# Kernel optimization log

Measured on AMD Instinct MI355X. Metric: run time of the kernel, lower is better.

## Reference

```python
import jax, jax.numpy as jnp
from jax import lax
import numpy as np

VOCAB, EMBED, HIDDEN, MEL = 256, 256, 1024, 80


def lstm_seq(x_seq, Wih, Whh, bih, bhh):
    """x_seq: [T, B, in]; returns hidden sequence [T, B, H]. PyTorch gate order i,f,g,o."""
    H = Whh.shape[1]
    B = x_seq.shape[1]
    b = bih + bhh

    def step(carry, x):
        h, c = carry
        g = x @ Wih.T + h @ Whh.T + b  # [B, 4H]
        i, f, gg, o = jnp.split(g, 4, axis=-1)
        c = jax.nn.sigmoid(f) * c + jax.nn.sigmoid(i) * jnp.tanh(gg)
        h = jax.nn.sigmoid(o) * jnp.tanh(c)
        return (h, c), h

    init = (jnp.zeros((B, H), x_seq.dtype), jnp.zeros((B, H), x_seq.dtype))
    _, ys = lax.scan(step, init, x_seq)
    return ys


def setup_inputs() -> dict:
    key = jax.random.key(0)
    ks = jax.random.split(key, 13)
    s_h = 1.0 / np.sqrt(HIDDEN)
    u = lambda k, shape, s: jax.random.uniform(k, shape, jnp.float32, -s, s)
    return {
        "text": jax.random.randint(ks[0], (64, 1024), 0, VOCAB),
        "text_lens": jax.random.randint(ks[1], (64,), 1, 1024),
        "max_audio_len": 1000,
        "W_emb": jax.random.normal(ks[2], (VOCAB, EMBED), jnp.float32),
        "enc_Wih": u(ks[3], (4 * HIDDEN, EMBED), s_h),
        "enc_Whh": u(ks[4], (4 * HIDDEN, HIDDEN), s_h),
        "enc_bih": u(ks[5], (4 * HIDDEN,), s_h),
        "enc_bhh": u(ks[6], (4 * HIDDEN,), s_h),
        "dec_Wih": u(ks[7], (4 * HIDDEN, MEL), s_h),
        "dec_Whh": u(ks[8], (4 * HIDDEN, HIDDEN), s_h),
        "dec_bih": u(ks[9], (4 * HIDDEN,), s_h),
        "dec_bhh": u(ks[10], (4 * HIDDEN,), s_h),
        "lin_W": u(ks[11], (MEL, HIDDEN), s_h),
        "lin_b": u(ks[12], (MEL,), s_h),
    }


def reference(text, text_lens, max_audio_len, W_emb, enc_Wih, enc_Whh, enc_bih,
              enc_bhh, dec_Wih, dec_Whh, dec_bih, dec_bhh, lin_W, lin_b):
    B = text.shape[0]
    # Encoder over text (output unused downstream, but computed as in the original).
    emb = W_emb[text]                      # [B, T, E]
    enc_out = lstm_seq(emb.transpose(1, 0, 2), enc_Wih, enc_Whh, enc_bih, enc_bhh)
    enc_out = enc_out.transpose(1, 0, 2)   # [B, T, H]

    b_dec = dec_bih + dec_bhh

    def dec_step(carry, _):
        h, c, x = carry                    # x: [B, MEL] previous frame
        g = x @ dec_Wih.T + h @ dec_Whh.T + b_dec
        i, f, gg, o = jnp.split(g, 4, axis=-1)
        c = jax.nn.sigmoid(f) * c + jax.nn.sigmoid(i) * jnp.tanh(gg)
        h = jax.nn.sigmoid(o) * jnp.tanh(c)
        frame = h @ lin_W.T + lin_b        # [B, MEL]
        return (h, c, frame), frame

    init = (jnp.zeros((B, HIDDEN), jnp.float32),
            jnp.zeros((B, HIDDEN), jnp.float32),
            jnp.zeros((B, MEL), jnp.float32))
    _, frames = lax.scan(dec_step, init, None, length=max_audio_len)
    return frames.transpose(1, 0, 2)       # [B, max_audio_len, MEL]
```

## Files before the change

kernel.cpp:

```cpp
#include <hip/hip_runtime.h>
#include <math.h>

#define HIDDEN 1024
#define MEL    80
#define TSTEPS 1000
#define BATCH  64

#define NBLK 64
#define TPB  1024

typedef unsigned long long ull;

__device__ __forceinline__ float sigm_f(float x) { return 1.0f / (1.0f + __expf(-x)); }
__device__ __forceinline__ float tanh_f(float x) { return 1.0f - 2.0f / (1.0f + __expf(2.0f * x)); }

__device__ __forceinline__ unsigned int pack_h(float h, int tag) {
    int q = (int)rintf(h * 8388608.0f);
    q = max(-8388607, min(8388607, q));
    return ((unsigned int)(tag & 0xFF) << 24) | ((unsigned int)q & 0xFFFFFFu);
}
__device__ __forceinline__ float unpack_h(unsigned int v) {
    int q = ((int)(v << 8)) >> 8;
    return (float)q * 1.1920928955078125e-7f;
}

__global__ __launch_bounds__(TPB, 4) void tts_recur(
    const float* __restrict__ dec_Wih,
    const float* __restrict__ dec_Whh,
    const float* __restrict__ dec_bih,
    const float* __restrict__ dec_bhh,
    const float* __restrict__ lin_W,
    const float* __restrict__ lin_b,
    float* __restrict__ h_hist,
    unsigned int* __restrict__ hbuf)
{
    const int tid  = threadIdx.x;
    const int blk  = blockIdx.x;
    const int wv   = tid >> 6;
    const int lane = tid & 63;
    const int jj   = lane & 15;
    const int gate = lane >> 4;
    const int unit_g = blk * 16 + jj;
    const int row_g  = gate * HIDDEN + unit_g;

    if (wv == 0) __builtin_amdgcn_s_setprio(3);

    __shared__ __align__(16) float hEx[16][64];
    __shared__ float part[2][64 * 17];

    const float* wih = dec_Wih + (size_t)row_g * MEL;
    const float* whh = dec_Whh + (size_t)row_g * HIDDEN + wv * 64;
    float4 w[16];
#pragma unroll
    for (int k = 0; k < 16; ++k)
        w[k] = *(const float4*)(whh + k * 4);
#pragma unroll 1
    for (int m = 0; m < MEL; ++m) {
        const float aw = wih[m];
        const float4* lw4 = (const float4*)(lin_W + (size_t)m * HIDDEN + wv * 64);
#pragma unroll
        for (int k = 0; k < 8; ++k) {
            const float4 lw = lw4[k];
            w[k].x = fmaf(aw, lw.x, w[k].x); w[k].y = fmaf(aw, lw.y, w[k].y);
            w[k].z = fmaf(aw, lw.z, w[k].z); w[k].w = fmaf(aw, lw.w, w[k].w);
        }
#pragma unroll
        for (int k = 8; k < 16; ++k) {
            const float4 lw = lw4[k];
            w[k].x = fmaf(aw, lw.x, w[k].x); w[k].y = fmaf(aw, lw.y, w[k].y);
            w[k].z = fmaf(aw, lw.z, w[k].z); w[k].w = fmaf(aw, lw.w, w[k].w);
        }
    }
    float b_comb_r = dec_bih[row_g] + dec_bhh[row_g];
    const float b_dec_r = b_comb_r;
    for (int m = 0; m < MEL; ++m)
        b_comb_r = fmaf(wih[m], lin_b[m], b_comb_r);

    float c_prev = 0.0f;

    if (wv == 0) {
        const float g = b_dec_r;
        const float gi = __shfl(g, jj, 64);
        const float gg = __shfl(g, 32 + jj, 64);
        const float go = __shfl(g, 48 + jj, 64);
        const float c  = sigm_f(gi) * tanh_f(gg);
        const float h  = sigm_f(go) * tanh_f(c);
        c_prev = c;
        if (lane < 16) {
            __hip_atomic_store(hbuf + unit_g, pack_h(h, 1),
                               __ATOMIC_RELAXED, __HIP_MEMORY_SCOPE_AGENT);
            h_hist[unit_g] = h;
        }
    }

    for (int t = 1; t < TSTEPS; ++t) {
        const int buf = t & 1;
        {
            const unsigned int* src = hbuf + ((t - 1) & 1) * HIDDEN;
            const unsigned int want = (unsigned int)t & 0xFFu;
            unsigned int v = __hip_atomic_load(src + tid, __ATOMIC_RELAXED, __HIP_MEMORY_SCOPE_AGENT);
            while ((v >> 24) != want)
                v = __hip_atomic_load(src + tid, __ATOMIC_RELAXED, __HIP_MEMORY_SCOPE_AGENT);
            hEx[wv][lane] = unpack_h(v);
        }
        __builtin_amdgcn_wave_barrier();

        const float4* hp = (const float4*)&hEx[wv][0];
        float a0 = 0.f, a1 = 0.f, a2 = 0.f, a3 = 0.f;
#pragma unroll
        for (int k = 0; k < 16; k += 4) {
            const float4 h0 = hp[k], h1 = hp[k + 1], h2 = hp[k + 2], h3 = hp[k + 3];
            a0 = fmaf(w[k].x, h0.x, a0);   a0 = fmaf(w[k].y, h0.y, a0);
            a0 = fmaf(w[k].z, h0.z, a0);   a0 = fmaf(w[k].w, h0.w, a0);
            a1 = fmaf(w[k+1].x, h1.x, a1); a1 = fmaf(w[k+1].y, h1.y, a1);
            a1 = fmaf(w[k+1].z, h1.z, a1); a1 = fmaf(w[k+1].w, h1.w, a1);
            a2 = fmaf(w[k+2].x, h2.x, a2); a2 = fmaf(w[k+2].y, h2.y, a2);
            a2 = fmaf(w[k+2].z, h2.z, a2); a2 = fmaf(w[k+2].w, h2.w, a2);
            a3 = fmaf(w[k+3].x, h3.x, a3); a3 = fmaf(w[k+3].y, h3.y, a3);
            a3 = fmaf(w[k+3].w, h3.w, a3); a3 = fmaf(w[k+3].z, h3.z, a3);
        }
        part[buf][lane * 17 + wv] = (a0 + a1) + (a2 + a3);
        __syncthreads();

        if (wv == 0) {
            const float* pr = &part[buf][lane * 17];
            float p[16];
#pragma unroll
            for (int i = 0; i < 16; ++i) p[i] = pr[i];
            const float s = (((p[0]+p[1])+(p[2]+p[3])) + ((p[4]+p[5])+(p[6]+p[7])))
                          + (((p[8]+p[9])+(p[10]+p[11])) + ((p[12]+p[13])+(p[14]+p[15])));
            const float g = s + b_comb_r;
            const float gi = __shfl(g, jj, 64);
            const float gf = __shfl(g, 16 + jj, 64);
            const float gg = __shfl(g, 32 + jj, 64);
            const float go = __shfl(g, 48 + jj, 64);
            const float c  = sigm_f(gf) * c_prev + sigm_f(gi) * tanh_f(gg);
            const float h  = sigm_f(go) * tanh_f(c);
            c_prev = c;
            if (lane < 16) {
                __hip_atomic_store(hbuf + buf * HIDDEN + unit_g, pack_h(h, t + 1),
                                   __ATOMIC_RELAXED, __HIP_MEMORY_SCOPE_AGENT);
                h_hist[(size_t)t * HIDDEN + unit_g] = h;
            }
        }
    }
}

__global__ __launch_bounds__(128) void tts_frames(
    const float* __restrict__ lin_W, const float* __restrict__ lin_b,
    const float* __restrict__ h_hist, float* __restrict__ out)
{
    const int t = blockIdx.x;
    const int tid = threadIdx.x;
    __shared__ __align__(16) float h_sh[HIDDEN];
    __shared__ float f_s[MEL];
    const float4* src = (const float4*)(h_hist + (size_t)t * HIDDEN);
    ((float4*)h_sh)[tid] = src[tid];
    ((float4*)h_sh)[tid + 128] = src[tid + 128];
    __syncthreads();
    if (tid < MEL) {
        const float* wrow = lin_W + (size_t)tid * HIDDEN;
        float acc = lin_b[tid];
#pragma unroll 8
        for (int c = 0; c < HIDDEN; ++c)
            acc = fmaf(wrow[c], h_sh[c], acc);
        f_s[tid] = acc;
    }
    __syncthreads();
    for (int idx = tid; idx < BATCH * MEL; idx += 128) {
        const int b = idx / MEL;
        const int m = idx - b * MEL;
        out[(size_t)b * TSTEPS * MEL + (size_t)t * MEL + m] = f_s[m];
    }
}

extern "C" void kernel_launch(void* const* d_in, const int* in_sizes, int n_in,
                              void* d_out, int out_size, void* d_ws, size_t ws_size,
                              hipStream_t stream) {
    const float* dec_Wih = (const float*)d_in[8];
    const float* dec_Whh = (const float*)d_in[9];
    const float* dec_bih = (const float*)d_in[10];
    const float* dec_bhh = (const float*)d_in[11];
    const float* lin_W   = (const float*)d_in[12];
    const float* lin_b   = (const float*)d_in[13];
    float* out = (float*)d_out;

    float* h_hist = (float*)d_ws;
    unsigned int* hbuf = (unsigned int*)((char*)d_ws + (size_t)TSTEPS * HIDDEN * sizeof(float));

    hipLaunchKernelGGL(tts_recur, dim3(NBLK), dim3(TPB), 0, stream,
                       dec_Wih, dec_Whh, dec_bih, dec_bhh, lin_W, lin_b, h_hist, hbuf);
    hipLaunchKernelGGL(tts_frames, dim3(TSTEPS), dim3(128), 0, stream,
                       lin_W, lin_b, h_hist, out);
}
```

Before: 2.304 ms.

## Split recurrent LSTM across 256 small blocks with 4 units each

Repartitions the persistent recurrent kernel from 64 blocks of 1024 threads (16 hidden units each) to 256 blocks of 256 threads (4 units each). Each thread still holds 64 Whh weights in registers, but each wave now covers 256 columns across 4 sub-groups. The h exchange now loads 4 packed values per thread via two 64-bit atomic loads into a padded shared buffer. The aim is to spread the work over more CUs and to shrink the per-block barrier and reduction. The cost is more blocks polling global memory for the tagged h values every step, which adds cross-block sync traffic.

```diff
diff --git a/kernel.cpp b/kernel.cpp
--- a/kernel.cpp
+++ b/kernel.cpp
@@ -6,8 +6,9 @@
 #define TSTEPS 1000
 #define BATCH  64
 
-#define NBLK 64
-#define TPB  1024
+#define NBLK 256
+#define TPB  256
+#define UPB  4
 
 typedef unsigned long long ull;
 
@@ -19,12 +20,14 @@
     q = max(-8388607, min(8388607, q));
     return ((unsigned int)(tag & 0xFF) << 24) | ((unsigned int)q & 0xFFFFFFu);
 }
-__device__ __forceinline__ float unpack_h(unsigned int v) {
+__device__ __forceinline__ float unpack_u(unsigned int v) {
     int q = ((int)(v << 8)) >> 8;
     return (float)q * 1.1920928955078125e-7f;
 }
 
-__global__ __launch_bounds__(TPB, 4) void tts_recur(
+__device__ __forceinline__ int hoff(int col) { return col + ((col >> 6) << 2); }
+
+__global__ __launch_bounds__(TPB) void tts_recur(
     const float* __restrict__ dec_Wih,
     const float* __restrict__ dec_Whh,
     const float* __restrict__ dec_bih,
@@ -38,18 +41,19 @@
     const int blk  = blockIdx.x;
     const int wv   = tid >> 6;
     const int lane = tid & 63;
-    const int jj   = lane & 15;
-    const int gate = lane >> 4;
-    const int unit_g = blk * 16 + jj;
-    const int row_g  = gate * HIDDEN + unit_g;
+    const int sub  = lane >> 4;
+    const int r16  = lane & 15;
+    const int unit0 = blk * UPB;
+    const int row_g = (r16 >> 2) * HIDDEN + unit0 + (r16 & 3);
+    const int colbase = wv * 256 + sub * 64;
 
     if (wv == 0) __builtin_amdgcn_s_setprio(3);
 
-    __shared__ __align__(16) float hEx[16][64];
-    __shared__ float part[2][64 * 17];
+    __shared__ __align__(16) float hEx[HIDDEN + 64];
+    __shared__ float part[2][16 * 17];
 
     const float* wih = dec_Wih + (size_t)row_g * MEL;
-    const float* whh = dec_Whh + (size_t)row_g * HIDDEN + wv * 64;
+    const float* whh = dec_Whh + (size_t)row_g * HIDDEN + colbase;
     float4 w[16];
 #pragma unroll
     for (int k = 0; k < 16; ++k)
@@ -57,7 +61,7 @@
 #pragma unroll 1
     for (int m = 0; m < MEL; ++m) {
         const float aw = wih[m];
-        const float4* lw4 = (const float4*)(lin_W + (size_t)m * HIDDEN + wv * 64);
+        const float4* lw4 = (const float4*)(lin_W + (size_t)m * HIDDEN + colbase);
 #pragma unroll
         for (int k = 0; k < 8; ++k) {
             const float4 lw = lw4[k];
@@ -80,32 +84,44 @@
 
     if (wv == 0) {
         const float g = b_dec_r;
-        const float gi = __shfl(g, jj, 64);
-        const float gg = __shfl(g, 32 + jj, 64);
-        const float go = __shfl(g, 48 + jj, 64);
+        const int j = lane & 3;
+        const float gi = __shfl(g, j, 64);
+        const float gg = __shfl(g, 8 + j, 64);
+        const float go = __shfl(g, 12 + j, 64);
         const float c  = sigm_f(gi) * tanh_f(gg);
         const float h  = sigm_f(go) * tanh_f(c);
         c_prev = c;
-        if (lane < 16) {
-            __hip_atomic_store(hbuf + unit_g, pack_h(h, 1),
+        if (lane < 4) {
+            __hip_atomic_store(hbuf + unit0 + lane, pack_h(h, 1),
                                __ATOMIC_RELAXED, __HIP_MEMORY_SCOPE_AGENT);
-            h_hist[unit_g] = h;
+            h_hist[unit0 + lane] = h;
         }
     }
 
     for (int t = 1; t < TSTEPS; ++t) {
         const int buf = t & 1;
         {
-            const unsigned int* src = hbuf + ((t - 1) & 1) * HIDDEN;
+            const ull* src = (const ull*)(hbuf + ((t - 1) & 1) * HIDDEN) + tid * 2;
             const unsigned int want = (unsigned int)t & 0xFFu;
-            unsigned int v = __hip_atomic_load(src + tid, __ATOMIC_RELAXED, __HIP_MEMORY_SCOPE_AGENT);
-            while ((v >> 24) != want)
-                v = __hip_atomic_load(src + tid, __ATOMIC_RELAXED, __HIP_MEMORY_SCOPE_AGENT);
-            hEx[wv][lane] = unpack_h(v);
+            ull a = __hip_atomic_load(src,     __ATOMIC_RELAXED, __HIP_MEMORY_SCOPE_AGENT);
+            ull b = __hip_atomic_load(src + 1, __ATOMIC_RELAXED, __HIP_MEMORY_SCOPE_AGENT);
+            while ((((unsigned)(a >> 24)) & 0xFFu) != want ||
+                   ((unsigned)(a >> 56))          != want ||
+                   (((unsigned)(b >> 24)) & 0xFFu) != want ||
+                   ((unsigned)(b >> 56))          != want) {
+                a = __hip_atomic_load(src,     __ATOMIC_RELAXED, __HIP_MEMORY_SCOPE_AGENT);
+                b = __hip_atomic_load(src + 1, __ATOMIC_RELAXED, __HIP_MEMORY_SCOPE_AGENT);
+            }
+            float4 hv;
+            hv.x = unpack_u((unsigned)a);
+            hv.y = unpack_u((unsigned)(a >> 32));
+            hv.z = unpack_u((unsigned)b);
+            hv.w = unpack_u((unsigned)(b >> 32));
+            *(float4*)&hEx[hoff(tid * 4)] = hv;
         }
         __builtin_amdgcn_wave_barrier();
 
-        const float4* hp = (const float4*)&hEx[wv][0];
+        const float4* hp = (const float4*)&hEx[hoff(colbase)];
         float a0 = 0.f, a1 = 0.f, a2 = 0.f, a3 = 0.f;
 #pragma unroll
         for (int k = 0; k < 16; k += 4) {
@@ -117,30 +133,34 @@
             a2 = fmaf(w[k+2].x, h2.x, a2); a2 = fmaf(w[k+2].y, h2.y, a2);
             a2 = fmaf(w[k+2].z, h2.z, a2); a2 = fmaf(w[k+2].w, h2.w, a2);
             a3 = fmaf(w[k+3].x, h3.x, a3); a3 = fmaf(w[k+3].y, h3.y, a3);
-            a3 = fmaf(w[k+3].w, h3.w, a3); a3 = fmaf(w[k+3].z, h3.z, a3);
-        }
-        part[buf][lane * 17 + wv] = (a0 + a1) + (a2 + a3);
+            a3 = fmaf(w[k+3].z, h3.z, a3); a3 = fmaf(w[k+3].w, h3.w, a3);
+        }
+        part[buf][r16 * 17 + (wv * 4 + sub)] = (a0 + a1) + (a2 + a3);
         __syncthreads();
 
         if (wv == 0) {
-            const float* pr = &part[buf][lane * 17];
-            float p[16];
-#pragma unroll
-            for (int i = 0; i < 16; ++i) p[i] = pr[i];
-            const float s = (((p[0]+p[1])+(p[2]+p[3])) + ((p[4]+p[5])+(p[6]+p[7])))
-                          + (((p[8]+p[9])+(p[10]+p[11])) + ((p[12]+p[13])+(p[14]+p[15])));
-            const float g = s + b_comb_r;
-            const float gi = __shfl(g, jj, 64);
-            const float gf = __shfl(g, 16 + jj, 64);
-            const float gg = __shfl(g, 32 + jj, 64);
-            const float go = __shfl(g, 48 + jj, 64);
+            float g = 0.0f;
+            if (lane < 16) {
+                const float* pr = &part[buf][lane * 17];
+                float p[16];
+#pragma unroll
+                for (int i = 0; i < 16; ++i) p[i] = pr[i];
+                const float s = (((p[0]+p[1])+(p[2]+p[3])) + ((p[4]+p[5])+(p[6]+p[7])))
+                              + (((p[8]+p[9])+(p[10]+p[11])) + ((p[12]+p[13])+(p[14]+p[15])));
+                g = s + b_comb_r;
+            }
+            const int j = lane & 3;
+            const float gi = __shfl(g, j, 64);
+            const float gf = __shfl(g, 4 + j, 64);
+            const float gg = __shfl(g, 8 + j, 64);
+            const float go = __shfl(g, 12 + j, 64);
             const float c  = sigm_f(gf) * c_prev + sigm_f(gi) * tanh_f(gg);
             const float h  = sigm_f(go) * tanh_f(c);
             c_prev = c;
-            if (lane < 16) {
-                __hip_atomic_store(hbuf + buf * HIDDEN + unit_g, pack_h(h, t + 1),
+            if (lane < 4) {
+                __hip_atomic_store(hbuf + buf * HIDDEN + unit0 + lane, pack_h(h, t + 1),
                                    __ATOMIC_RELAXED, __HIP_MEMORY_SCOPE_AGENT);
-                h_hist[(size_t)t * HIDDEN + unit_g] = h;
+                h_hist[(size_t)t * HIDDEN + unit0 + lane] = h;
             }
         }
     }
```

Result: slower. 3.174 ms (+37.7%).

## Repartition recurrence to 32 blocks of 32 units with register+LDS weight split

Applied to the files above, without the earlier changes.

Restructures the persistent recurrence kernel. Instead of 64 blocks of 1024 threads each owning 16 units, it launches 256 blocks, keeps only every eighth one alive (32 active blocks), and gives each 512-thread block 32 hidden units. Each thread covers one gate row and a 256-column slice, holding 192 weights in registers and 64 in LDS. The hidden-state poll now uses two 64-bit loads per lane, and the final reduction is over 4 partials instead of 16. The aim is fewer cross-block synchronisation participants and fewer reduction partials per step. In exchange there is more per-thread serial FMA work per step, higher register pressure, and extra idle blocks that launch and exit immediately.

```diff
diff --git a/kernel.cpp b/kernel.cpp
--- a/kernel.cpp
+++ b/kernel.cpp
@@ -6,8 +6,11 @@
 #define TSTEPS 1000
 #define BATCH  64
 
-#define NBLK 64
-#define TPB  1024
+#define NBLK 256
+#define TPB  512
+#define UPB  32
+#define VREG 48
+#define LCH  16
 
 typedef unsigned long long ull;
 
@@ -19,12 +22,12 @@
     q = max(-8388607, min(8388607, q));
     return ((unsigned int)(tag & 0xFF) << 24) | ((unsigned int)q & 0xFFFFFFu);
 }
-__device__ __forceinline__ float unpack_h(unsigned int v) {
+__device__ __forceinline__ float unpack_u(unsigned int v) {
     int q = ((int)(v << 8)) >> 8;
     return (float)q * 1.1920928955078125e-7f;
 }
 
-__global__ __launch_bounds__(TPB, 4) void tts_recur(
+__global__ __launch_bounds__(TPB, 2) void tts_recur(
     const float* __restrict__ dec_Wih,
     const float* __restrict__ dec_Whh,
     const float* __restrict__ dec_bih,
@@ -34,82 +37,120 @@
     float* __restrict__ h_hist,
     unsigned int* __restrict__ hbuf)
 {
+    if (blockIdx.x & 7) return;
+    const int W    = blockIdx.x >> 3;
     const int tid  = threadIdx.x;
-    const int blk  = blockIdx.x;
     const int wv   = tid >> 6;
     const int lane = tid & 63;
-    const int jj   = lane & 15;
-    const int gate = lane >> 4;
-    const int unit_g = blk * 16 + jj;
-    const int row_g  = gate * HIDDEN + unit_g;
-
-    if (wv == 0) __builtin_amdgcn_s_setprio(3);
-
-    __shared__ __align__(16) float hEx[16][64];
-    __shared__ float part[2][64 * 17];
-
-    const float* wih = dec_Wih + (size_t)row_g * MEL;
-    const float* whh = dec_Whh + (size_t)row_g * HIDDEN + wv * 64;
-    float4 w[16];
-#pragma unroll
-    for (int k = 0; k < 16; ++k)
-        w[k] = *(const float4*)(whh + k * 4);
+    const int row  = tid & 127;
+    const int cg   = tid >> 7;
+    const int unit0 = W * UPB;
+    const int row_g = (row & 3) * HIDDEN + unit0 + (row >> 2);
+    const int colbase = cg * 256;
+
+    __shared__ __align__(16) float wlds[LCH * TPB * 4];
+    __shared__ __align__(16) float hEx[8][256];
+    __shared__ float part[2][128 * 5];
+
+    const float*  wih  = dec_Wih + (size_t)row_g * MEL;
+    const float4* whh4 = (const float4*)(dec_Whh + (size_t)row_g * HIDDEN + colbase);
+    float* lrow = (float*)hEx;
+
+    {
+        float4 t[LCH];
+#pragma unroll
+        for (int c = 0; c < LCH; ++c) t[c] = whh4[VREG + c];
+#pragma unroll 1
+        for (int m = 0; m < MEL; ++m) {
+            __syncthreads();
+            *(float2*)&lrow[tid * 2] = *(const float2*)(lin_W + (size_t)m * HIDDEN + tid * 2);
+            __syncthreads();
+            const float aw = wih[m];
+            const float4* lw4 = (const float4*)&lrow[colbase];
+#pragma unroll
+            for (int c = 0; c < LCH; ++c) {
+                const float4 lw = lw4[VREG + c];
+                t[c].x = fmaf(aw, lw.x, t[c].x); t[c].y = fmaf(aw, lw.y, t[c].y);
+                t[c].z = fmaf(aw, lw.z, t[c].z); t[c].w = fmaf(aw, lw.w, t[c].w);
+            }
+        }
+#pragma unroll
+        for (int c = 0; c < LCH; ++c)
+            ((float4*)wlds)[c * TPB + tid] = t[c];
+    }
+    float4 w[VREG];
+#pragma unroll
+    for (int k = 0; k < VREG; ++k) w[k] = whh4[k];
 #pragma unroll 1
     for (int m = 0; m < MEL; ++m) {
+        __syncthreads();
+        *(float2*)&lrow[tid * 2] = *(const float2*)(lin_W + (size_t)m * HIDDEN + tid * 2);
+        __syncthreads();
         const float aw = wih[m];
-        const float4* lw4 = (const float4*)(lin_W + (size_t)m * HIDDEN + wv * 64);
-#pragma unroll
-        for (int k = 0; k < 8; ++k) {
+        const float4* lw4 = (const float4*)&lrow[colbase];
+#pragma unroll
+        for (int k = 0; k < VREG; ++k) {
             const float4 lw = lw4[k];
             w[k].x = fmaf(aw, lw.x, w[k].x); w[k].y = fmaf(aw, lw.y, w[k].y);
             w[k].z = fmaf(aw, lw.z, w[k].z); w[k].w = fmaf(aw, lw.w, w[k].w);
         }
-#pragma unroll
-        for (int k = 8; k < 16; ++k) {
-            const float4 lw = lw4[k];
-            w[k].x = fmaf(aw, lw.x, w[k].x); w[k].y = fmaf(aw, lw.y, w[k].y);
-            w[k].z = fmaf(aw, lw.z, w[k].z); w[k].w = fmaf(aw, lw.w, w[k].w);
-        }
-    }
-    float b_comb_r = dec_bih[row_g] + dec_bhh[row_g];
-    const float b_dec_r = b_comb_r;
-    for (int m = 0; m < MEL; ++m)
-        b_comb_r = fmaf(wih[m], lin_b[m], b_comb_r);
-
-    float c_prev = 0.0f;
-
-    if (wv == 0) {
-        const float g = b_dec_r;
-        const float gi = __shfl(g, jj, 64);
-        const float gg = __shfl(g, 32 + jj, 64);
-        const float go = __shfl(g, 48 + jj, 64);
+    }
+    __syncthreads();
+
+    float b_comb = 0.0f, b_dec = 0.0f, c_prev = 0.0f;
+    if (tid < 128) {
+        float b = dec_bih[row_g] + dec_bhh[row_g];
+        b_dec = b;
+        for (int m = 0; m < MEL; ++m)
+            b = fmaf(wih[m], lin_b[m], b);
+        b_comb = b;
+    }
+
+    if (tid < 128) {
+        const float g  = b_dec;
+        const int   bl = lane & 60;
+        const float gi = __shfl(g, bl, 64);
+        const float gg = __shfl(g, bl | 2, 64);
+        const float go = __shfl(g, bl | 3, 64);
         const float c  = sigm_f(gi) * tanh_f(gg);
         const float h  = sigm_f(go) * tanh_f(c);
         c_prev = c;
-        if (lane < 16) {
-            __hip_atomic_store(hbuf + unit_g, pack_h(h, 1),
+        if ((lane & 3) == 0) {
+            const int slot = unit0 + (row >> 2);
+            __hip_atomic_store(hbuf + slot, pack_h(h, 1),
                                __ATOMIC_RELAXED, __HIP_MEMORY_SCOPE_AGENT);
-            h_hist[unit_g] = h;
+            h_hist[slot] = h;
         }
     }
 
     for (int t = 1; t < TSTEPS; ++t) {
         const int buf = t & 1;
         {
-            const unsigned int* src = hbuf + ((t - 1) & 1) * HIDDEN;
+            const ull* src8 = (const ull*)(hbuf + ((t - 1) & 1) * HIDDEN)
+                              + (cg * 128 + lane * 2);
             const unsigned int want = (unsigned int)t & 0xFFu;
-            unsigned int v = __hip_atomic_load(src + tid, __ATOMIC_RELAXED, __HIP_MEMORY_SCOPE_AGENT);
-            while ((v >> 24) != want)
-                v = __hip_atomic_load(src + tid, __ATOMIC_RELAXED, __HIP_MEMORY_SCOPE_AGENT);
-            hEx[wv][lane] = unpack_h(v);
+            ull a  = __hip_atomic_load(src8,     __ATOMIC_RELAXED, __HIP_MEMORY_SCOPE_AGENT);
+            ull b8 = __hip_atomic_load(src8 + 1, __ATOMIC_RELAXED, __HIP_MEMORY_SCOPE_AGENT);
+            while ((((unsigned)(a  >> 24)) & 0xFFu) != want ||
+                   ((unsigned)(a  >> 56))           != want ||
+                   (((unsigned)(b8 >> 24)) & 0xFFu) != want ||
+                   ((unsigned)(b8 >> 56))           != want) {
+                a  = __hip_atomic_load(src8,     __ATOMIC_RELAXED, __HIP_MEMORY_SCOPE_AGENT);
+                b8 = __hip_atomic_load(src8 + 1, __ATOMIC_RELAXED, __HIP_MEMORY_SCOPE_AGENT);
+            }
+            float4 hv;
+            hv.x = unpack_u((unsigned)a);        hv.y = unpack_u((unsigned)(a >> 32));
+            hv.z = unpack_u((unsigned)b8);       hv.w = unpack_u((unsigned)(b8 >> 32));
+            *(float4*)&hEx[wv][lane * 4] = hv;
         }
         __builtin_amdgcn_wave_barrier();
 
         const float4* hp = (const float4*)&hEx[wv][0];
+        const float4* wl = (const float4*)wlds;
         float a0 = 0.f, a1 = 0.f, a2 = 0.f, a3 = 0.f;
 #pragma unroll
-        for (int k = 0; k < 16; k += 4) {
-            const float4 h0 = hp[k], h1 = hp[k + 1], h2 = hp[k + 2], h3 = hp[k + 3];
+        for (int k = 0; k < VREG; k += 4) {
+            const float4 h0 = hp[k], h1 = hp[k+1], h2 = hp[k+2], h3 = hp[k+3];
             a0 = fmaf(w[k].x, h0.x, a0);   a0 = fmaf(w[k].y, h0.y, a0);
             a0 = fmaf(w[k].z, h0.z, a0);   a0 = fmaf(w[k].w, h0.w, a0);
             a1 = fmaf(w[k+1].x, h1.x, a1); a1 = fmaf(w[k+1].y, h1.y, a1);
@@ -117,30 +158,42 @@
             a2 = fmaf(w[k+2].x, h2.x, a2); a2 = fmaf(w[k+2].y, h2.y, a2);
             a2 = fmaf(w[k+2].z, h2.z, a2); a2 = fmaf(w[k+2].w, h2.w, a2);
             a3 = fmaf(w[k+3].x, h3.x, a3); a3 = fmaf(w[k+3].y, h3.y, a3);
-            a3 = fmaf(w[k+3].w, h3.w, a3); a3 = fmaf(w[k+3].z, h3.z, a3);
-        }
-        part[buf][lane * 17 + wv] = (a0 + a1) + (a2 + a3);
+            a3 = fmaf(w[k+3].z, h3.z, a3); a3 = fmaf(w[k+3].w, h3.w, a3);
+        }
+#pragma unroll
+        for (int c = 0; c < LCH; c += 4) {
+            const float4 h0 = hp[VREG+c], h1 = hp[VREG+c+1],
+                         h2 = hp[VREG+c+2], h3 = hp[VREG+c+3];
+            const float4 u0 = wl[c*TPB + tid],     u1 = wl[(c+1)*TPB + tid],
+                         u2 = wl[(c+2)*TPB + tid], u3 = wl[(c+3)*TPB + tid];
+            a0 = fmaf(u0.x, h0.x, a0); a0 = fmaf(u0.y, h0.y, a0);
+            a0 = fmaf(u0.z, h0.z, a0); a0 = fmaf(u0.w, h0.w, a0);
+            a1 = fmaf(u1.x, h1.x, a1); a1 = fmaf(u1.y, h1.y, a1);
+            a1 = fmaf(u1.z, h1.z, a1); a1 = fmaf(u1.w, h1.w, a1);
+            a2 = fmaf(u2.x, h2.x, a2); a2 = fmaf(u2.y, h2.y, a2);
+            a2 = fmaf(u2.z, h2.z, a2); a2 = fmaf(u2.w, h2.w, a2);
+            a3 = fmaf(u3.x, h3.x, a3); a3 = fmaf(u3.y, h3.y, a3);
+            a3 = fmaf(u3.z, h3.z, a3); a3 = fmaf(u3.w, h3.w, a3);
+        }
+        part[buf][row * 5 + cg] = (a0 + a1) + (a2 + a3);
         __syncthreads();
 
-        if (wv == 0) {
-            const float* pr = &part[buf][lane * 17];
-            float p[16];
-#pragma unroll
-            for (int i = 0; i < 16; ++i) p[i] = pr[i];
-            const float s = (((p[0]+p[1])+(p[2]+p[3])) + ((p[4]+p[5])+(p[6]+p[7])))
-                          + (((p[8]+p[9])+(p[10]+p[11])) + ((p[12]+p[13])+(p[14]+p[15])));
-            const float g = s + b_comb_r;
-            const float gi = __shfl(g, jj, 64);
-            const float gf = __shfl(g, 16 + jj, 64);
-            const float gg = __shfl(g, 32 + jj, 64);
-            const float go = __shfl(g, 48 + jj, 64);
+        if (tid < 128) {
+            const float* pr = &part[buf][row * 5];
+            const float g  = ((pr[0] + pr[1]) + (pr[2] + pr[3])) + b_comb;
+            const int   bl = lane & 60;
+            const float gi = __shfl(g, bl, 64);
+            const float gf = __shfl(g, bl | 1, 64);
+            const float gg = __shfl(g, bl | 2, 64);
+            const float go = __shfl(g, bl | 3, 64);
             const float c  = sigm_f(gf) * c_prev + sigm_f(gi) * tanh_f(gg);
             const float h  = sigm_f(go) * tanh_f(c);
             c_prev = c;
-            if (lane < 16) {
-                __hip_atomic_store(hbuf + buf * HIDDEN + unit_g, pack_h(h, t + 1),
+            if ((lane & 3) == 0) {
+                const int slot = unit0 + (row >> 2);
+                __hip_atomic_store(hbuf + buf * HIDDEN + slot, pack_h(h, t + 1),
                                    __ATOMIC_RELAXED, __HIP_MEMORY_SCOPE_AGENT);
-                h_hist[(size_t)t * HIDDEN + unit_g] = h;
+                h_hist[(size_t)t * HIDDEN + slot] = h;
             }
         }
     }
```

New measurement: 3.474 ms. 1.51x slower.
